# Kernel tuning notes

Measured on AMD Instinct MI355X. Metric: run time of the kernel, lower is better.

The kernel has to match this reference:

```python
import jax, jax.numpy as jnp
import numpy as np

CODEBOOK_SIZE = 512
LATENT_DIM = 12
BATCH = 512
TOKENS = 256


def setup_inputs() -> dict:
    key = jax.random.key(0)
    k1, k2 = jax.random.split(key)
    x = jax.random.normal(k1, (BATCH, TOKENS, LATENT_DIM), dtype=jnp.float32)
    # nn.Embedding init: uniform(-1/K, 1/K)
    lim = 1.0 / CODEBOOK_SIZE
    codebook = jax.random.uniform(k2, (CODEBOOK_SIZE, LATENT_DIM), dtype=jnp.float32,
                                  minval=-lim, maxval=lim)
    return {"x": x, "codebook": codebook}


def reference(x, codebook):
    # same as for torch.cdist (sqrt is monotonic).
    x2 = jnp.sum(x * x, axis=-1, keepdims=True)            # [B, N, 1]
    w2 = jnp.sum(codebook * codebook, axis=-1)             # [K]
    xw = jnp.einsum('bnd,kd->bnk', x, codebook)            # [B, N, K]
    dist2 = x2 - 2.0 * xw + w2                             # [B, N, K]
    indices = jnp.argmin(dist2, axis=-1)                   # [B, N] int
    quantized = codebook[indices]                          # [B, N, D]

    codebook_loss = jnp.mean((quantized - jax.lax.stop_gradient(x)) ** 2)
    commitment_loss = 0.25 * jnp.mean((jax.lax.stop_gradient(quantized) - x) ** 2)
    quantize_loss = codebook_loss + commitment_loss

    # straight-through estimator
    quantized_st = x + jax.lax.stop_gradient(quantized - x)
    return quantized_st, indices, quantize_loss
```

## Files before the change

kernel.cpp:

```cpp
#include <hip/hip_runtime.h>
#include <math.h>

namespace {
constexpr int KCB   = 512;
constexpr int DIM   = 12;
constexpr int NTOK  = 512 * 256;
constexpr int QSIZE = NTOK * DIM;
constexpr int NSPLIT = 8;
constexpr int KCHUNK = KCB / NSPLIT;
constexpr int TPT    = 2;
constexpr int TOKS_PER_BLOCK = 64 * TPT;
constexpr int NBLK   = NTOK / TOKS_PER_BLOCK;
constexpr int ROWF   = 16;

typedef __attribute__((ext_vector_type(16))) float f32x16;

__device__ inline float code_score_s(const float (&xv)[DIM], float x2,
                                     const f32x16& r) {
    float xw = 0.f;
    xw = fmaf(xv[0],  r[0],  xw);
    xw = fmaf(xv[1],  r[1],  xw);
    xw = fmaf(xv[2],  r[2],  xw);
    xw = fmaf(xv[3],  r[3],  xw);
    xw = fmaf(xv[4],  r[4],  xw);
    xw = fmaf(xv[5],  r[5],  xw);
    xw = fmaf(xv[6],  r[6],  xw);
    xw = fmaf(xv[7],  r[7],  xw);
    xw = fmaf(xv[8],  r[8],  xw);
    xw = fmaf(xv[9],  r[9],  xw);
    xw = fmaf(xv[10], r[10], xw);
    xw = fmaf(xv[11], r[11], xw);
    return fmaf(-2.f, xw, x2) + r[12];
}

__device__ inline unsigned long long mkkey(float v, int k) {
    unsigned su = __float_as_uint(v);
    su = (su & 0x80000000u) ? ~su : (su | 0x80000000u);
    return ((unsigned long long)su << 32) | (unsigned)k;
}

__global__ __launch_bounds__(256) void pack_cb(const float* __restrict__ cb,
                                               float* __restrict__ pk,
                                               float* __restrict__ out) {
    int k = blockIdx.x * blockDim.x + threadIdx.x;
    if (k == 0) out[QSIZE + NTOK] = 0.f;
    if (k >= KCB) return;
    float w[DIM];
#pragma unroll
    for (int d = 0; d < DIM; ++d) w[d] = cb[k * DIM + d];
    float w2 = 0.f;
#pragma unroll
    for (int d = 0; d < DIM; ++d) w2 = fmaf(w[d], w[d], w2);
#pragma unroll
    for (int d = 0; d < DIM; ++d) pk[k * ROWF + d] = w[d];
    pk[k * ROWF + 12] = w2;
    pk[k * ROWF + 13] = 0.f; pk[k * ROWF + 14] = 0.f; pk[k * ROWF + 15] = 0.f;
    if (k == KCB - 1) {
#pragma unroll
        for (int d = 0; d < ROWF; ++d) pk[KCB * ROWF + d] = 0.f;
    }
}

__global__ __launch_bounds__(512, 4) void vq_main(const float* __restrict__ x,
                                                  const float* __restrict__ cb,
                                                  const float* __restrict__ pk,
                                                  float* __restrict__ out) {
    __shared__ unsigned long long keys[NSPLIT * TOKS_PER_BLOCK];
    __shared__ float lred[TPT];
    const int tid  = threadIdx.x;
    const int lane = tid & 63;
    const int s = __builtin_amdgcn_readfirstlane(tid >> 6);
    const int tbase = blockIdx.x * TOKS_PER_BLOCK;

    float xs[TPT][DIM];
    float x2[TPT];
#pragma unroll
    for (int j = 0; j < TPT; ++j) {
        const float4* xp = (const float4*)(x + (size_t)(tbase + j * 64 + lane) * DIM);
        float4 a0 = xp[0], a1 = xp[1], a2 = xp[2];
        xs[j][0] = a0.x; xs[j][1] = a0.y; xs[j][2]  = a0.z; xs[j][3]  = a0.w;
        xs[j][4] = a1.x; xs[j][5] = a1.y; xs[j][6]  = a1.z; xs[j][7]  = a1.w;
        xs[j][8] = a2.x; xs[j][9] = a2.y; xs[j][10] = a2.z; xs[j][11] = a2.w;
        float t2 = 0.f;
#pragma unroll
        for (int d = 0; d < DIM; ++d) t2 = fmaf(xs[j][d], xs[j][d], t2);
        x2[j] = t2;
    }

    float best[TPT];
    int   bi[TPT];
#pragma unroll
    for (int j = 0; j < TPT; ++j) { best[j] = INFINITY; bi[j] = 0; }

    const int k0 = s * KCHUNK;
    unsigned long long cwa = (unsigned long long)(pk + (size_t)k0 * ROWF);

    f32x16 A, B;
    asm volatile("s_load_dwordx16 %0, %1, 0" : "=s"(A) : "s"(cwa));
    asm volatile("s_waitcnt lgkmcnt(0)" : "+s"(A));
#pragma unroll
    for (int kk = 0; kk < KCHUNK; kk += 2) {
        asm volatile("s_load_dwordx16 %0, %1, 0"
                     : "=s"(B) : "s"(cwa + (unsigned long long)((kk + 1) * 64)));
        {
            const int k = k0 + kk;
#pragma unroll
            for (int j = 0; j < TPT; ++j) {
                float d = code_score_s(xs[j], x2[j], A);
                bool c = d < best[j];
                best[j] = c ? d : best[j];
                bi[j]   = c ? k : bi[j];
            }
        }
        asm volatile("s_waitcnt lgkmcnt(0)" : "+s"(B));
        asm volatile("s_load_dwordx16 %0, %1, 0"
                     : "=s"(A) : "s"(cwa + (unsigned long long)((kk + 2) * 64)));
        {
            const int k = k0 + kk + 1;
#pragma unroll
            for (int j = 0; j < TPT; ++j) {
                float d = code_score_s(xs[j], x2[j], B);
                bool c = d < best[j];
                best[j] = c ? d : best[j];
                bi[j]   = c ? k : bi[j];
            }
        }
        asm volatile("s_waitcnt lgkmcnt(0)" : "+s"(A));
    }

#pragma unroll
    for (int j = 0; j < TPT; ++j)
        keys[s * TOKS_PER_BLOCK + j * 64 + lane] = mkkey(best[j], bi[j]);
    __syncthreads();

    if (s < TPT) {
        const int tok = s * 64 + lane;
        unsigned long long m = keys[tok];
#pragma unroll
        for (int r = 1; r < NSPLIT; ++r) {
            unsigned long long v = keys[r * TOKS_PER_BLOCK + tok];
            m = v < m ? v : m;
        }
        const int bid = (int)(m & 0xffffffffULL);
        unsigned eu = (unsigned)(m >> 32);
        unsigned orig = (eu & 0x80000000u) ? (eu ^ 0x80000000u) : ~eu;
        const float bsc = __uint_as_float(orig);
        const int t = tbase + tok;

        float xv[DIM];
#pragma unroll
        for (int j = 0; j < TPT; ++j)
            if (j == s) {
#pragma unroll
                for (int d = 0; d < DIM; ++d) xv[d] = xs[j][d];
            }

        const float4* wrow = (const float4*)(cb + (size_t)bid * DIM);
        float4 q0 = wrow[0], q1 = wrow[1], q2 = wrow[2];
        float qs[DIM] = {q0.x, q0.y, q0.z, q0.w, q1.x, q1.y, q1.z, q1.w,
                         q2.x, q2.y, q2.z, q2.w};

        float4* qo = (float4*)(out + (size_t)t * DIM);
        float4 r0, r1, r2;
        r0.x = xv[0] + (qs[0] - xv[0]);    r0.y = xv[1] + (qs[1] - xv[1]);
        r0.z = xv[2] + (qs[2] - xv[2]);    r0.w = xv[3] + (qs[3] - xv[3]);
        r1.x = xv[4] + (qs[4] - xv[4]);    r1.y = xv[5] + (qs[5] - xv[5]);
        r1.z = xv[6] + (qs[6] - xv[6]);    r1.w = xv[7] + (qs[7] - xv[7]);
        r2.x = xv[8] + (qs[8] - xv[8]);    r2.y = xv[9] + (qs[9] - xv[9]);
        r2.z = xv[10] + (qs[10] - xv[10]); r2.w = xv[11] + (qs[11] - xv[11]);
        qo[0] = r0; qo[1] = r1; qo[2] = r2;

        out[QSIZE + t] = (float)bid;

        float ls = bsc * (1.25f / (float)QSIZE);
#pragma unroll
        for (int off = 32; off > 0; off >>= 1) ls += __shfl_down(ls, off);
        if (lane == 0) lred[s] = ls;
    }
    __syncthreads();
    if (tid == 0) atomicAdd(out + QSIZE + NTOK, lred[0] + lred[1]);
}
}

extern "C" void kernel_launch(void* const* d_in, const int* in_sizes, int n_in,
                              void* d_out, int out_size, void* d_ws, size_t ws_size,
                              hipStream_t stream) {
    const float* x  = (const float*)d_in[0];
    const float* cb = (const float*)d_in[1];
    float* out = (float*)d_out;
    float* pk  = (float*)d_ws;

    pack_cb<<<2, 256, 0, stream>>>(cb, pk, out);
    vq_main<<<NBLK, 512, 0, stream>>>(x, cb, pk, out);
}
```

Measured before the change: 102.2 us.

## Broadcast codewords from registers via readlane and process four tokens per thread

Each wave loads its 64-code chunk of the codebook into per-lane registers, computes norms in-kernel, and broadcasts each codeword with readlane instead of streaming a packed codebook through scalar loads. This removes the separate packing kernel and the scalar memory latency chain. Tokens per thread double to 4, halving blocks and amortizing broadcasts, at the cost of more VGPRs and 13 readlane ops per code.

```diff
diff --git a/kernel.cpp b/kernel.cpp
--- a/kernel.cpp
+++ b/kernel.cpp
@@ -8,30 +8,9 @@
 constexpr int QSIZE = NTOK * DIM;
 constexpr int NSPLIT = 8;
 constexpr int KCHUNK = KCB / NSPLIT;
-constexpr int TPT    = 2;
+constexpr int TPT    = 4;
 constexpr int TOKS_PER_BLOCK = 64 * TPT;
 constexpr int NBLK   = NTOK / TOKS_PER_BLOCK;
-constexpr int ROWF   = 16;
-
-typedef __attribute__((ext_vector_type(16))) float f32x16;
-
-__device__ inline float code_score_s(const float (&xv)[DIM], float x2,
-                                     const f32x16& r) {
-    float xw = 0.f;
-    xw = fmaf(xv[0],  r[0],  xw);
-    xw = fmaf(xv[1],  r[1],  xw);
-    xw = fmaf(xv[2],  r[2],  xw);
-    xw = fmaf(xv[3],  r[3],  xw);
-    xw = fmaf(xv[4],  r[4],  xw);
-    xw = fmaf(xv[5],  r[5],  xw);
-    xw = fmaf(xv[6],  r[6],  xw);
-    xw = fmaf(xv[7],  r[7],  xw);
-    xw = fmaf(xv[8],  r[8],  xw);
-    xw = fmaf(xv[9],  r[9],  xw);
-    xw = fmaf(xv[10], r[10], xw);
-    xw = fmaf(xv[11], r[11], xw);
-    return fmaf(-2.f, xw, x2) + r[12];
-}
 
 __device__ inline unsigned long long mkkey(float v, int k) {
     unsigned su = __float_as_uint(v);
@@ -39,31 +18,16 @@
     return ((unsigned long long)su << 32) | (unsigned)k;
 }
 
-__global__ __launch_bounds__(256) void pack_cb(const float* __restrict__ cb,
-                                               float* __restrict__ pk,
-                                               float* __restrict__ out) {
-    int k = blockIdx.x * blockDim.x + threadIdx.x;
-    if (k == 0) out[QSIZE + NTOK] = 0.f;
-    if (k >= KCB) return;
-    float w[DIM];
-#pragma unroll
-    for (int d = 0; d < DIM; ++d) w[d] = cb[k * DIM + d];
-    float w2 = 0.f;
-#pragma unroll
-    for (int d = 0; d < DIM; ++d) w2 = fmaf(w[d], w[d], w2);
-#pragma unroll
-    for (int d = 0; d < DIM; ++d) pk[k * ROWF + d] = w[d];
-    pk[k * ROWF + 12] = w2;
-    pk[k * ROWF + 13] = 0.f; pk[k * ROWF + 14] = 0.f; pk[k * ROWF + 15] = 0.f;
-    if (k == KCB - 1) {
-#pragma unroll
-        for (int d = 0; d < ROWF; ++d) pk[KCB * ROWF + d] = 0.f;
-    }
+__device__ inline float bcast(float v, int lane) {
+    return __uint_as_float(__builtin_amdgcn_readlane(__float_as_uint(v), lane));
+}
+
+__global__ void init_loss(float* __restrict__ out) {
+    if (threadIdx.x == 0) out[QSIZE + NTOK] = 0.f;
 }
 
 __global__ __launch_bounds__(512, 4) void vq_main(const float* __restrict__ x,
                                                   const float* __restrict__ cb,
-                                                  const float* __restrict__ pk,
                                                   float* __restrict__ out) {
     __shared__ unsigned long long keys[NSPLIT * TOKS_PER_BLOCK];
     __shared__ float lred[TPT];
@@ -71,6 +35,20 @@
     const int lane = tid & 63;
     const int s = __builtin_amdgcn_readfirstlane(tid >> 6);
     const int tbase = blockIdx.x * TOKS_PER_BLOCK;
+
+    float cw[13];
+    {
+        const int kc = (s << 6) + lane;
+        const float4* wp = (const float4*)(cb + (size_t)kc * DIM);
+        float4 c0 = wp[0], c1 = wp[1], c2 = wp[2];
+        cw[0] = c0.x; cw[1] = c0.y; cw[2]  = c0.z; cw[3]  = c0.w;
+        cw[4] = c1.x; cw[5] = c1.y; cw[6]  = c1.z; cw[7]  = c1.w;
+        cw[8] = c2.x; cw[9] = c2.y; cw[10] = c2.z; cw[11] = c2.w;
+        float w2 = 0.f;
+#pragma unroll
+        for (int d = 0; d < DIM; ++d) w2 = fmaf(cw[d], cw[d], w2);
+        cw[12] = w2;
+    }
 
     float xs[TPT][DIM];
     float x2[TPT];
@@ -92,40 +70,34 @@
 #pragma unroll
     for (int j = 0; j < TPT; ++j) { best[j] = INFINITY; bi[j] = 0; }
 
-    const int k0 = s * KCHUNK;
-    unsigned long long cwa = (unsigned long long)(pk + (size_t)k0 * ROWF);
+    const int k0 = s << 6;
 
-    f32x16 A, B;
-    asm volatile("s_load_dwordx16 %0, %1, 0" : "=s"(A) : "s"(cwa));
-    asm volatile("s_waitcnt lgkmcnt(0)" : "+s"(A));
+#pragma unroll 8
+    for (int kk = 0; kk < KCHUNK; ++kk) {
+        float w[13];
 #pragma unroll
-    for (int kk = 0; kk < KCHUNK; kk += 2) {
-        asm volatile("s_load_dwordx16 %0, %1, 0"
-                     : "=s"(B) : "s"(cwa + (unsigned long long)((kk + 1) * 64)));
-        {
-            const int k = k0 + kk;
+        for (int d = 0; d < 13; ++d) w[d] = bcast(cw[d], kk);
+        const int k = k0 + kk;
 #pragma unroll
-            for (int j = 0; j < TPT; ++j) {
-                float d = code_score_s(xs[j], x2[j], A);
-                bool c = d < best[j];
-                best[j] = c ? d : best[j];
-                bi[j]   = c ? k : bi[j];
-            }
+        for (int j = 0; j < TPT; ++j) {
+            float xw = 0.f;
+            xw = fmaf(xs[j][0],  w[0],  xw);
+            xw = fmaf(xs[j][1],  w[1],  xw);
+            xw = fmaf(xs[j][2],  w[2],  xw);
+            xw = fmaf(xs[j][3],  w[3],  xw);
+            xw = fmaf(xs[j][4],  w[4],  xw);
+            xw = fmaf(xs[j][5],  w[5],  xw);
+            xw = fmaf(xs[j][6],  w[6],  xw);
+            xw = fmaf(xs[j][7],  w[7],  xw);
+            xw = fmaf(xs[j][8],  w[8],  xw);
+            xw = fmaf(xs[j][9],  w[9],  xw);
+            xw = fmaf(xs[j][10], w[10], xw);
+            xw = fmaf(xs[j][11], w[11], xw);
+            float d = fmaf(-2.f, xw, x2[j]) + w[12];
+            bool c = d < best[j];
+            best[j] = c ? d : best[j];
+            bi[j]   = c ? k : bi[j];
         }
-        asm volatile("s_waitcnt lgkmcnt(0)" : "+s"(B));
-        asm volatile("s_load_dwordx16 %0, %1, 0"
-                     : "=s"(A) : "s"(cwa + (unsigned long long)((kk + 2) * 64)));
-        {
-            const int k = k0 + kk + 1;
-#pragma unroll
-            for (int j = 0; j < TPT; ++j) {
-                float d = code_score_s(xs[j], x2[j], B);
-                bool c = d < best[j];
-                best[j] = c ? d : best[j];
-                bi[j]   = c ? k : bi[j];
-            }
-        }
-        asm volatile("s_waitcnt lgkmcnt(0)" : "+s"(A));
     }
 
 #pragma unroll
@@ -178,7 +150,7 @@
         if (lane == 0) lred[s] = ls;
     }
     __syncthreads();
-    if (tid == 0) atomicAdd(out + QSIZE + NTOK, lred[0] + lred[1]);
+    if (tid == 0) atomicAdd(out + QSIZE + NTOK, lred[0] + lred[1] + lred[2] + lred[3]);
 }
 }
 
@@ -188,8 +160,8 @@
     const float* x  = (const float*)d_in[0];
     const float* cb = (const float*)d_in[1];
     float* out = (float*)d_out;
-    float* pk  = (float*)d_ws;
+    (void)d_ws; (void)ws_size;
 
-    pack_cb<<<2, 256, 0, stream>>>(cb, pk, out);
-    vq_main<<<NBLK, 512, 0, stream>>>(x, cb, pk, out);
+    init_loss<<<1, 64, 0, stream>>>(out);
+    vq_main<<<NBLK, 512, 0, stream>>>(x, cb, out);
 }
```

New measurement: 95.97 us. 1.06x faster.
